# Performance work log

Measured on AMD Instinct MI355X. Metric: run time of the kernel, lower is better.

The kernel has to match this reference:

```python
import jax, jax.numpy as jnp
import numpy as np

MAX_HOP = 3

def setup_inputs() -> dict:
    key = jax.random.key(0)
    k1, k2, k3 = jax.random.split(key, 3)
    B, M, D = 8, 8192, 256
    query_vector = jax.random.normal(k1, (B, D), dtype=jnp.float32)
    global_pointer = jax.random.uniform(k2, (B, M), dtype=jnp.float32)  # sigmoid-range
    m_story = jax.random.normal(k3, (MAX_HOP + 1, B, M, D), dtype=jnp.float32) * 0.1
    return {"query_vector": query_vector, "global_pointer": global_pointer, "m_story": m_story}


def reference(query_vector, global_pointer, m_story):
    # query_vector: [B, D]; global_pointer: [B, M]; m_story: [H+1, B, M, D]
    u = query_vector
    gp = global_pointer[:, :, None]  # [B, M, 1]
    prob_soft = None
    prob_logits = None
    for hop in range(MAX_HOP):
        m_A = m_story[hop] * gp                       # [B, M, D] pointer gating
        prob_logits = jnp.einsum('bmd,bd->bm', m_A, u)  # broadcast mul + sum over D
        prob_soft = jax.nn.softmax(prob_logits, axis=1)  # softmax over memory dim
        m_C = m_story[hop + 1] * gp                   # [B, M, D]
        o_k = jnp.einsum('bm,bmd->bd', prob_soft, m_C)  # weighted sum over memory
        u = u + o_k
    return (prob_soft, prob_logits)
```

## Files before the change

kernel.cpp:

```cpp
#include <hip/hip_runtime.h>
#include <hip/hip_bf16.h>

#define B 8
#define M 8192
#define D 256
#define BM (B * M)
#define BMD ((size_t)B * M * D)

__global__ __launch_bounds__(256) void logits_kernel(
    const float* __restrict__ story,
    const float* __restrict__ u,
    const float* __restrict__ gp,
    float* __restrict__ logits,
    float* __restrict__ psum,
    const float* __restrict__ ucopy_src,
    float* __restrict__ ucopy_dst)
{
    if (ucopy_dst != nullptr && blockIdx.x < 8)
        ucopy_dst[blockIdx.x * 256 + threadIdx.x] =
            ucopy_src[blockIdx.x * 256 + threadIdx.x];

    const int lane = threadIdx.x & 63;
    const int wv   = threadIdx.x >> 6;
    const long long row0 = ((long long)blockIdx.x * 4 + wv) * 8;
    const int b = (int)(row0 >> 13);
    __shared__ float sred[4];

    const float4 uf = reinterpret_cast<const float4*>(u + b * D)[lane];
    const float4* srow = reinterpret_cast<const float4*>(story + row0 * D) + lane;

    float esum = 0.f;
    #pragma unroll
    for (int r = 0; r < 8; ++r) {
        float4 s = srow[(size_t)r * 64];
        float v = s.x * uf.x + s.y * uf.y + s.z * uf.z + s.w * uf.w;
        #pragma unroll
        for (int off = 32; off; off >>= 1) v += __shfl_xor(v, off, 64);
        if (lane == 0) {
            float l = v * gp[row0 + r];
            logits[row0 + r] = l;
            esum += __expf(l);
        }
    }
    if (lane == 0) sred[wv] = esum;
    __syncthreads();
    if (threadIdx.x == 0)
        psum[(b << 8) + (blockIdx.x & 255)] = sred[0] + sred[1] + sred[2] + sred[3];
}

__global__ __launch_bounds__(256) void ok_kernel(
    const float* __restrict__ story,
    const float* __restrict__ gp,
    const float* __restrict__ logits,
    const float* __restrict__ psum,
    float* __restrict__ u_out)
{
    const int bid = blockIdx.x;
    const int b = bid >> 7, c = bid & 127;
    const int tid = threadIdx.x, lane = tid & 63, wv = tid >> 6;
    __shared__ float red[256];
    __shared__ float w[64];
    __shared__ float sacc[4][256];

    red[tid] = psum[(b << 8) + tid];
    __syncthreads();
    for (int s = 128; s; s >>= 1) {
        if (tid < s) red[tid] += red[tid + s];
        __syncthreads();
    }
    const float inv_denom = 1.f / red[0];

    const long long row0 = (long long)b * M + (long long)c * 64;
    if (tid < 64)
        w[tid] = __expf(logits[row0 + tid]) * inv_denom * gp[row0 + tid];
    __syncthreads();

    float4 acc = {0.f, 0.f, 0.f, 0.f};
    const float4* s4 = reinterpret_cast<const float4*>(story + row0 * D) + lane;
    #pragma unroll
    for (int r = 0; r < 16; ++r) {
        const int row = (wv << 4) + r;
        float4 s = s4[(size_t)row * 64];
        const float ww = w[row];
        acc.x += ww * s.x; acc.y += ww * s.y; acc.z += ww * s.z; acc.w += ww * s.w;
    }
    reinterpret_cast<float4*>(&sacc[wv][0])[lane] = acc;
    __syncthreads();
    const float out = sacc[0][tid] + sacc[1][tid] + sacc[2][tid] + sacc[3][tid];
    atomicAdd(&u_out[b * D + tid], out);
}

__global__ __launch_bounds__(256) void prob_kernel(
    const float* __restrict__ logits,
    const float* __restrict__ psum,
    float* __restrict__ prob)
{
    const int tid = threadIdx.x;
    const int b = blockIdx.x >> 5;
    __shared__ float red[256];
    red[tid] = psum[(b << 8) + tid];
    __syncthreads();
    for (int s = 128; s; s >>= 1) {
        if (tid < s) red[tid] += red[tid + s];
        __syncthreads();
    }
    const float inv = 1.f / red[0];
    const int i = blockIdx.x * 256 + tid;
    prob[i] = __expf(logits[i]) * inv;
}

extern "C" void kernel_launch(void* const* d_in, const int* in_sizes, int n_in,
                              void* d_out, int out_size, void* d_ws, size_t ws_size,
                              hipStream_t stream) {
    const float* query = (const float*)d_in[0];
    const float* gp    = (const float*)d_in[1];
    const float* story = (const float*)d_in[2];

    float* out    = (float*)d_out;
    float* prob   = out;
    float* logits = out + BM;

    float* ws   = (float*)d_ws;
    float* u1   = ws;
    float* u2   = ws + 2048;
    float* psum = ws + 4096;

    const float* st0 = story;
    const float* st1 = story + BMD;
    const float* st2 = story + 2 * BMD;

    logits_kernel<<<BM / 32, 256, 0, stream>>>(st0, query, gp, logits, psum,
                                               query, u1);
    ok_kernel<<<B * 128, 256, 0, stream>>>(st1, gp, logits, psum, u1);

    logits_kernel<<<BM / 32, 256, 0, stream>>>(st1, u1, gp, logits, psum,
                                               u1, u2);
    ok_kernel<<<B * 128, 256, 0, stream>>>(st2, gp, logits, psum, u2);

    logits_kernel<<<BM / 32, 256, 0, stream>>>(st2, u2, gp, logits, psum,
                                               nullptr, nullptr);
    prob_kernel<<<BM / 256, 256, 0, stream>>>(logits, psum, prob);
}
```

Baseline: 71.71 us.

## Fuse logits and weighted-sum per hop using unnormalized softmax accumulation

Merges the logits and o_k kernels into one hop kernel. Each block computes exp-weighted partial sums of the next story slice and atomically accumulates both the numerator and the softmax denominator. The normalization is deferred to the next hop, which rebuilds u from query plus numerator over denominator, so there is no separate reduction pass and no logits round-trip between kernels. Intermediate hops also skip writing logits. This drops kernel launches and extra global traffic, but adds a memset and relies on exp without max subtraction, which could overflow for large logits.

```diff
diff --git a/kernel.cpp b/kernel.cpp
--- a/kernel.cpp
+++ b/kernel.cpp
@@ -7,87 +7,78 @@
 #define BM (B * M)
 #define BMD ((size_t)B * M * D)
 
-__global__ __launch_bounds__(256) void logits_kernel(
-    const float* __restrict__ story,
-    const float* __restrict__ u,
+__global__ __launch_bounds__(256) void hop_kernel(
+    const float* __restrict__ st_h,
+    const float* __restrict__ st_next,
+    const float* __restrict__ query,
     const float* __restrict__ gp,
-    float* __restrict__ logits,
-    float* __restrict__ psum,
-    const float* __restrict__ ucopy_src,
-    float* __restrict__ ucopy_dst)
+    const float* __restrict__ on0, const float* __restrict__ z0,
+    const float* __restrict__ on1, const float* __restrict__ z1,
+    float* __restrict__ onum_out,
+    float* __restrict__ z_out,
+    float* __restrict__ logits_out,
+    float* __restrict__ psum_out)
 {
-    if (ucopy_dst != nullptr && blockIdx.x < 8)
-        ucopy_dst[blockIdx.x * 256 + threadIdx.x] =
-            ucopy_src[blockIdx.x * 256 + threadIdx.x];
+    const int bid = blockIdx.x;
+    const int b = bid >> 7;
+    const int tid = threadIdx.x, lane = tid & 63, wv = tid >> 6;
+    const long long grow0 = (long long)bid * 64;
 
-    const int lane = threadIdx.x & 63;
-    const int wv   = threadIdx.x >> 6;
-    const long long row0 = ((long long)blockIdx.x * 4 + wv) * 8;
-    const int b = (int)(row0 >> 13);
+    __shared__ float uu[256];
+    __shared__ float gpv[64];
+    __shared__ float w[64];
     __shared__ float sred[4];
+    __shared__ float sacc[4][256];
 
-    const float4 uf = reinterpret_cast<const float4*>(u + b * D)[lane];
-    const float4* srow = reinterpret_cast<const float4*>(story + row0 * D) + lane;
+    float uq = query[b * 256 + tid];
+    if (on0) uq += on0[b * 256 + tid] / z0[b];
+    if (on1) uq += on1[b * 256 + tid] / z1[b];
+    uu[tid] = uq;
+    if (tid < 64) gpv[tid] = gp[grow0 + tid];
+    __syncthreads();
 
+    const float4 uf = reinterpret_cast<const float4*>(uu)[lane];
+
+    const float4* s1 = reinterpret_cast<const float4*>(st_h + grow0 * D) + lane;
     float esum = 0.f;
     #pragma unroll
-    for (int r = 0; r < 8; ++r) {
-        float4 s = srow[(size_t)r * 64];
+    for (int r = 0; r < 16; ++r) {
+        const int row = (wv << 4) + r;
+        float4 s = s1[(size_t)row * 64];
         float v = s.x * uf.x + s.y * uf.y + s.z * uf.z + s.w * uf.w;
         #pragma unroll
         for (int off = 32; off; off >>= 1) v += __shfl_xor(v, off, 64);
         if (lane == 0) {
-            float l = v * gp[row0 + r];
-            logits[row0 + r] = l;
-            esum += __expf(l);
+            const float g = gpv[row];
+            const float l = v * g;
+            const float e = __expf(l);
+            esum += e;
+            w[row] = e * g;
+            if (logits_out) logits_out[grow0 + row] = l;
         }
     }
     if (lane == 0) sred[wv] = esum;
     __syncthreads();
-    if (threadIdx.x == 0)
-        psum[(b << 8) + (blockIdx.x & 255)] = sred[0] + sred[1] + sred[2] + sred[3];
-}
 
-__global__ __launch_bounds__(256) void ok_kernel(
-    const float* __restrict__ story,
-    const float* __restrict__ gp,
-    const float* __restrict__ logits,
-    const float* __restrict__ psum,
-    float* __restrict__ u_out)
-{
-    const int bid = blockIdx.x;
-    const int b = bid >> 7, c = bid & 127;
-    const int tid = threadIdx.x, lane = tid & 63, wv = tid >> 6;
-    __shared__ float red[256];
-    __shared__ float w[64];
-    __shared__ float sacc[4][256];
+    if (st_next == nullptr) {
+        if (tid == 0) psum_out[bid] = sred[0] + sred[1] + sred[2] + sred[3];
+        return;
+    }
 
-    red[tid] = psum[(b << 8) + tid];
-    __syncthreads();
-    for (int s = 128; s; s >>= 1) {
-        if (tid < s) red[tid] += red[tid + s];
-        __syncthreads();
-    }
-    const float inv_denom = 1.f / red[0];
-
-    const long long row0 = (long long)b * M + (long long)c * 64;
-    if (tid < 64)
-        w[tid] = __expf(logits[row0 + tid]) * inv_denom * gp[row0 + tid];
-    __syncthreads();
-
+    const float4* s2 = reinterpret_cast<const float4*>(st_next + grow0 * D) + lane;
     float4 acc = {0.f, 0.f, 0.f, 0.f};
-    const float4* s4 = reinterpret_cast<const float4*>(story + row0 * D) + lane;
     #pragma unroll
     for (int r = 0; r < 16; ++r) {
         const int row = (wv << 4) + r;
-        float4 s = s4[(size_t)row * 64];
+        float4 s = s2[(size_t)row * 64];
         const float ww = w[row];
         acc.x += ww * s.x; acc.y += ww * s.y; acc.z += ww * s.z; acc.w += ww * s.w;
     }
     reinterpret_cast<float4*>(&sacc[wv][0])[lane] = acc;
     __syncthreads();
-    const float out = sacc[0][tid] + sacc[1][tid] + sacc[2][tid] + sacc[3][tid];
-    atomicAdd(&u_out[b * D + tid], out);
+    const float o = sacc[0][tid] + sacc[1][tid] + sacc[2][tid] + sacc[3][tid];
+    atomicAdd(&onum_out[b * 256 + tid], o);
+    if (tid == 0) atomicAdd(z_out + b, sred[0] + sred[1] + sred[2] + sred[3]);
 }
 
 __global__ __launch_bounds__(256) void prob_kernel(
@@ -97,10 +88,10 @@
 {
     const int tid = threadIdx.x;
     const int b = blockIdx.x >> 5;
-    __shared__ float red[256];
-    red[tid] = psum[(b << 8) + tid];
+    __shared__ float red[128];
+    if (tid < 128) red[tid] = psum[b * 128 + tid];
     __syncthreads();
-    for (int s = 128; s; s >>= 1) {
+    for (int s = 64; s; s >>= 1) {
         if (tid < s) red[tid] += red[tid + s];
         __syncthreads();
     }
@@ -121,23 +112,26 @@
     float* logits = out + BM;
 
     float* ws   = (float*)d_ws;
-    float* u1   = ws;
-    float* u2   = ws + 2048;
-    float* psum = ws + 4096;
+    float* on0  = ws;
+    float* z0   = ws + 2048;
+    float* on1  = ws + 2048 + 8;
+    float* z1   = ws + 4096 + 8;
+    float* psum = ws + 4104;
 
     const float* st0 = story;
     const float* st1 = story + BMD;
     const float* st2 = story + 2 * BMD;
 
-    logits_kernel<<<BM / 32, 256, 0, stream>>>(st0, query, gp, logits, psum,
-                                               query, u1);
-    ok_kernel<<<B * 128, 256, 0, stream>>>(st1, gp, logits, psum, u1);
+    hipMemsetAsync(ws, 0, 4112 * sizeof(float), stream);
 
-    logits_kernel<<<BM / 32, 256, 0, stream>>>(st1, u1, gp, logits, psum,
-                                               u1, u2);
-    ok_kernel<<<B * 128, 256, 0, stream>>>(st2, gp, logits, psum, u2);
-
-    logits_kernel<<<BM / 32, 256, 0, stream>>>(st2, u2, gp, logits, psum,
-                                               nullptr, nullptr);
+    hop_kernel<<<BM / 64, 256, 0, stream>>>(st0, st1, query, gp,
+                                            nullptr, nullptr, nullptr, nullptr,
+                                            on0, z0, nullptr, nullptr);
+    hop_kernel<<<BM / 64, 256, 0, stream>>>(st1, st2, query, gp,
+                                            on0, z0, nullptr, nullptr,
+                                            on1, z1, nullptr, nullptr);
+    hop_kernel<<<BM / 64, 256, 0, stream>>>(st2, nullptr, query, gp,
+                                            on0, z0, on1, z1,
+                                            nullptr, nullptr, logits, psum);
     prob_kernel<<<BM / 256, 256, 0, stream>>>(logits, psum, prob);
 }
```

New measurement: 86.16 us. +20.2%, slower.
